# Kernel tuning notes

Hardware: AMD Instinct MI355X
Metric: run time of the kernel (lower is better)

## Reference

```python
import jax, jax.numpy as jnp
import numpy as np

TEMP = 0.02
KD_W = 1.0
VSD_W = 1.0
VLAD_W = 1.0
CON_W = 1.0
MSE_W = 1.0

B, SS, ST, DS, DT, V, NV, NT = 8, 96, 128, 1024, 2048, 32000, 32, 64


def hungarian(cost):
    # Shortest-augmenting-path assignment (e-maxx / Jonker-Volgenant style).
    # Square cost [n, n]; returns col_of_row so that row i matches column
    # col_of_row[i] with minimal total cost (same as scipy linear_sum_assignment).
    cost = np.asarray(cost, dtype=np.float64)
    n = cost.shape[0]
    INF = 1e18
    u = np.zeros(n + 1)
    v = np.zeros(n + 1)
    p = np.zeros(n + 1, dtype=np.int64)
    way = np.zeros(n + 1, dtype=np.int64)
    for i in range(1, n + 1):
        p[0] = i
        j0 = 0
        minv = np.full(n + 1, INF)
        used = np.zeros(n + 1, dtype=bool)
        while True:
            used[j0] = True
            i0 = p[j0]
            js = np.nonzero(~used)[0]
            js = js[js > 0]
            cur = cost[i0 - 1, js - 1] - u[i0] - v[js]
            upd = cur < minv[js]
            minv[js] = np.where(upd, cur, minv[js])
            way[js] = np.where(upd, j0, way[js])
            k = int(np.argmin(minv[js]))
            delta = minv[js][k]
            j1 = int(js[k])
            u[p[used]] += delta
            v[used] -= delta
            minv[~used] -= delta
            j0 = j1
            if p[j0] == 0:
                break
        while j0:
            j1 = int(way[j0])
            p[j0] = p[j1]
            j0 = j1
    col_of_row = np.zeros(n, dtype=np.int64)
    for j in range(1, n + 1):
        col_of_row[p[j] - 1] = j - 1
    return col_of_row


def _match(s_logits, t_logits):
    # Per-sample L1 (p=1 cdist) cost between teacher rows and student cols,
    # then Hungarian matching. Host-side loop is unavoidable (sequential
    # combinatorial algorithm), matching the original per-sample scipy loop.
    idx = []
    for b in range(s_logits.shape[0]):
        cost = np.abs(t_logits[b][:, None, :] - s_logits[b][None, :, :]).sum(-1)
        idx.append(hungarian(cost))
    return np.stack(idx)


def _cosine(a, b, eps=1e-8):
    # a: [B, M, D], b: [B, N, D] -> [B, M, N]; torch F.cosine_similarity semantics
    an = a / jnp.maximum(jnp.linalg.norm(a, axis=-1, keepdims=True), eps)
    bn = b / jnp.maximum(jnp.linalg.norm(b, axis=-1, keepdims=True), eps)
    return jnp.einsum('bmd,bnd->bmn', an, bn)


def setup_inputs() -> dict:
    key = jax.random.key(0)
    ks = jax.random.split(key, 12)
    f = jax.random.normal
    return {
        's_qry_reps': f(ks[0], (B, DS), jnp.float32),
        's_pos_reps': f(ks[1], (B, DS), jnp.float32),
        't_qry_reps': f(ks[2], (B, DT), jnp.float32),
        't_pos_reps': f(ks[3], (B, DT), jnp.float32),
        's_hidden_qry': f(ks[4], (B, SS, DS), jnp.float32),
        's_hidden_pos': f(ks[5], (B, SS, DS), jnp.float32),
        't_hidden_qry': f(ks[6], (B, ST, DT), jnp.float32),
        't_hidden_pos': f(ks[7], (B, ST, DT), jnp.float32),
        'W_s_lm': f(ks[8], (DS, V), jnp.float32) / np.float32(np.sqrt(DS)),
        'W_t_lm': f(ks[9], (DT, V), jnp.float32) / np.float32(np.sqrt(DT)),
        'W_proj': f(ks[10], (DT, DS), jnp.float32) / np.float32(np.sqrt(DT)),
        'b_proj': jnp.zeros((DS,), jnp.float32),
        'nv': NV,
        'nt': NT,
    }


def reference(s_qry_reps, s_pos_reps, t_qry_reps, t_pos_reps,
              s_hidden_qry, s_hidden_pos, t_hidden_qry, t_hidden_pos,
              W_s_lm, W_t_lm, W_proj, b_proj, nv, nt):
    Bn = s_qry_reps.shape[0]
    # 1) contrastive InfoNCE (world_size=1 -> gather is identity, target=arange)
    scores = (s_qry_reps @ s_pos_reps.T) / TEMP
    logp = jax.nn.log_softmax(scores, axis=-1)
    contrastive = -jnp.mean(jnp.diagonal(logp))
    # 2) MSE vs t2s-projected teacher reps
    mse = 0.5 * (jnp.mean((s_qry_reps - (t_qry_reps @ W_proj + b_proj)) ** 2)
                 + jnp.mean((s_pos_reps - (t_pos_reps @ W_proj + b_proj)) ** 2))
    # 3/4) VSD + VLAD over qry and pos sides stacked -> [2B, ...]
    s_hid = jnp.concatenate([s_hidden_qry, s_hidden_pos], axis=0)
    t_hid = jnp.concatenate([t_hidden_qry, t_hidden_pos], axis=0)
    St = t_hid.shape[1]
    sv = s_hid[:, :nv]                      # student vision tokens   [2B, Nv, DS]
    st = s_hid[:, nv:nv + nt]               # student text tokens     [2B, Nt, DS]
    tv = t_hid[:, St - nv - nt:St - nt]     # teacher vision tokens   [2B, Nv, DT]
    tt = t_hid[:, St - nt:]                 # teacher text tokens     [2B, Nt, DT]
    s_logits = jnp.einsum('bnd,dv->bnv', sv, W_s_lm)   # [2B, Nv, V]
    t_logits = jnp.einsum('bnd,dv->bnv', tv, W_t_lm)   # [2B, Nv, V]
    # Hungarian matching on detached logits (host side, like the original)
    idx = jnp.asarray(_match(np.asarray(s_logits), np.asarray(t_logits)))  # [2B, Nv]
    # VSD: MSE between matched student logits and teacher logits (t order = arange)
    s_logits_m = jnp.take_along_axis(s_logits, idx[:, :, None], axis=1)
    vsd = jnp.sum(jnp.mean((s_logits_m - t_logits) ** 2, axis=(1, 2)))
    # VLAD: smooth-L1 on vision->text cosine affinity maps
    sv_m = jnp.take_along_axis(sv, idx[:, :, None], axis=1)
    d = _cosine(sv_m, st) - _cosine(tv, tt)            # [2B, Nv, Nt]
    ad = jnp.abs(d)
    sl1 = jnp.where(ad < 1.0, 0.5 * d * d, ad - 0.5)
    vlad = jnp.sum(jnp.mean(sl1, axis=(1, 2)))
    distill = (VSD_W * vsd + VLAD_W * vlad) / Bn
    loss = CON_W * contrastive + MSE_W * mse + KD_W * distill
    return loss, contrastive, distill
```

## Files before the change

kernel.cpp:

```cpp
#include <hip/hip_runtime.h>
#include <math.h>

#define DS_ 1024
#define DT_ 2048
#define V_  32000
#define SS_ 96
#define ST_ 128


__device__ __forceinline__ float block_reduce_sum_256(float v) {
  __shared__ float tmp[4];
  #pragma unroll
  for (int off = 32; off; off >>= 1) v += __shfl_xor(v, off);
  const int wid = threadIdx.x >> 6;
  if ((threadIdx.x & 63) == 0) tmp[wid] = v;
  __syncthreads();
  if (threadIdx.x == 0) v = tmp[0] + tmp[1] + tmp[2] + tmp[3];
  return v;
}

__device__ __forceinline__ const float* s_base(int b, const float* s_hq, const float* s_hp) {
  return (b < 8) ? (s_hq + (size_t)b * SS_ * DS_) : (s_hp + (size_t)(b - 8) * SS_ * DS_);
}
__device__ __forceinline__ const float* t_base(int b, const float* t_hq, const float* t_hp) {
  return (b < 8) ? (t_hq + (size_t)b * ST_ * DT_) : (t_hp + (size_t)(b - 8) * ST_ * DT_);
}

__device__ __forceinline__ unsigned short f2bf(float x) {
  unsigned int u = __float_as_uint(x);
  u += 0x7fffu + ((u >> 16) & 1u);
  return (unsigned short)(u >> 16);
}
__device__ __forceinline__ float bf2f(unsigned short u) {
  return __uint_as_float(((unsigned int)u) << 16);
}

using bf16x8 = __attribute__((ext_vector_type(8))) short;
using f32x4  = __attribute__((ext_vector_type(4))) float;
using u16x4  = __attribute__((ext_vector_type(4))) unsigned short;

__device__ __forceinline__ void gll16(const void* g, void* l) {
  __builtin_amdgcn_global_load_lds((const __attribute__((address_space(1))) unsigned int*)g,
                                   (__attribute__((address_space(3))) unsigned int*)l, 16, 0, 0);
}

__device__ __forceinline__ unsigned int wave_umin_dpp(unsigned int r) {
  unsigned int t;
  t = (unsigned int)__builtin_amdgcn_update_dpp((int)r, (int)r, 0x111, 0xF, 0xF, false); r = r < t ? r : t;
  t = (unsigned int)__builtin_amdgcn_update_dpp((int)r, (int)r, 0x112, 0xF, 0xF, false); r = r < t ? r : t;
  t = (unsigned int)__builtin_amdgcn_update_dpp((int)r, (int)r, 0x114, 0xF, 0xF, false); r = r < t ? r : t;
  t = (unsigned int)__builtin_amdgcn_update_dpp((int)r, (int)r, 0x118, 0xF, 0xF, false); r = r < t ? r : t;
  t = (unsigned int)__builtin_amdgcn_update_dpp((int)r, (int)r, 0x142, 0xF, 0xF, false); r = r < t ? r : t;
  t = (unsigned int)__builtin_amdgcn_update_dpp((int)r, (int)r, 0x143, 0xF, 0xF, false); r = r < t ? r : t;
  return r;
}


__device__ __forceinline__ void scores_body(int blk, const float* __restrict__ sq,
                                            const float* __restrict__ sp,
                                            float* __restrict__ scores) {
  const int i = blk >> 3, j = blk & 7;
  float acc = 0.f;
  for (int k = threadIdx.x; k < DS_; k += 256)
    acc += sq[(size_t)i * DS_ + k] * sp[(size_t)j * DS_ + k];
  acc = block_reduce_sum_256(acc);
  if (threadIdx.x == 0) scores[i * 8 + j] = acc * 50.0f;
}

__device__ __forceinline__ void proj2_body(int kc, const float* __restrict__ t_qry,
                                           const float* __restrict__ t_pos,
                                           const float* __restrict__ Wp,
                                           float* __restrict__ proj,
                                           unsigned char* smem) {
  float (*tv)[64] = (float (*)[64])smem;
  const int tid = threadIdx.x;
  for (int s = tid; s < 16 * 64; s += 256) {
    const int zi = s >> 6, k = s & 63;
    const float* t = (zi >= 8) ? (t_pos + (size_t)(zi - 8) * DT_) : (t_qry + (size_t)zi * DT_);
    tv[zi][k] = t[kc * 64 + k];
  }
  __syncthreads();
  const int d4 = tid * 4;
  float4 acc[16];
  #pragma unroll
  for (int zi = 0; zi < 16; ++zi) acc[zi] = (float4){0.f, 0.f, 0.f, 0.f};
  for (int k = 0; k < 64; ++k) {
    const float4 w = *(const float4*)&Wp[(size_t)(kc * 64 + k) * DS_ + d4];
    #pragma unroll
    for (int zi = 0; zi < 16; ++zi) {
      const float t = tv[zi][k];
      acc[zi].x += t * w.x; acc[zi].y += t * w.y;
      acc[zi].z += t * w.z; acc[zi].w += t * w.w;
    }
  }
  #pragma unroll
  for (int zi = 0; zi < 16; ++zi) {
    float* p = proj + (size_t)zi * DS_ + d4;
    atomicAdd(&p[0], acc[zi].x); atomicAdd(&p[1], acc[zi].y);
    atomicAdd(&p[2], acc[zi].z); atomicAdd(&p[3], acc[zi].w);
  }
}

__device__ __forceinline__ void norms_body(int blk, const float* __restrict__ s_hq,
                                           const float* __restrict__ s_hp,
                                           const float* __restrict__ t_hq,
                                           const float* __restrict__ t_hp,
                                           float* __restrict__ invn) {
  const int b = blk / 192, t = blk % 192;
  const float* bs = s_base(b, s_hq, s_hp);
  const float* bt = t_base(b, t_hq, t_hp);
  const float* row;
  int K;
  float* out;
  if (t < 32)       { row = bs + (size_t)t * DS_;             K = DS_; out = invn + b * 32 + t; }
  else if (t < 96)  { row = bs + (size_t)t * DS_;             K = DS_; out = invn + 512 + b * 64 + (t - 32); }
  else if (t < 128) { row = bt + (size_t)(t - 96 + 32) * DT_;  K = DT_; out = invn + 1536 + b * 32 + (t - 96); }
  else              { row = bt + (size_t)(t - 128 + 64) * DT_; K = DT_; out = invn + 2048 + b * 64 + (t - 128); }
  float ss = 0.f;
  for (int k = threadIdx.x; k < K; k += 256) { const float x = row[k]; ss += x * x; }
  ss = block_reduce_sum_256(ss);
  if (threadIdx.x == 0) *out = 1.0f / fmaxf(sqrtf(ss), 1e-8f);
}

__device__ __forceinline__ void pack_as_body(int g, const float* __restrict__ s_hq,
                                             const float* __restrict__ s_hp,
                                             unsigned short* __restrict__ As) {
  const int b = g >> 5, i = g & 31;
  const float* src = s_base(b, s_hq, s_hp) + (size_t)i * DS_;
  const int k4 = threadIdx.x * 4;
  const float4 w = *(const float4*)&src[k4];
  u16x4 o; o[0] = f2bf(w.x); o[1] = f2bf(w.y); o[2] = f2bf(w.z); o[3] = f2bf(w.w);
  *(u16x4*)&As[(size_t)g * DS_ + k4] = o;
}

__device__ __forceinline__ void pack_at_body(int g, const float* __restrict__ t_hq,
                                             const float* __restrict__ t_hp,
                                             unsigned short* __restrict__ At) {
  const int b = g >> 5, i = g & 31;
  const float* src = t_base(b, t_hq, t_hp) + (size_t)(32 + i) * DT_;
  #pragma unroll
  for (int it = 0; it < 2; ++it) {
    const int k4 = (threadIdx.x + it * 256) * 4;
    const float4 w = *(const float4*)&src[k4];
    u16x4 o; o[0] = f2bf(w.x); o[1] = f2bf(w.y); o[2] = f2bf(w.z); o[3] = f2bf(w.w);
    *(u16x4*)&At[(size_t)g * DT_ + k4] = o;
  }
}

__device__ __forceinline__ void convw3_body(int id, const float* __restrict__ W,
                                            unsigned short* __restrict__ Wbt,
                                            int K, unsigned char* smem) {
  float* tile = (float*)smem;
  const int v0 = (id % 250) * 128, k0 = (id / 250) * 64;
  const int tid = threadIdx.x;
  const int wv = tid >> 6, lane = tid & 63;
  const int rowsel = lane >> 5, vlane = lane & 31;
  #pragma unroll
  for (int it = 0; it < 8; ++it) {
    const int w = it * 4 + wv;
    gll16(W + (size_t)(k0 + 2 * w + rowsel) * V_ + v0 + vlane * 4,
          tile + w * 256);
  }
  __syncthreads();
  #pragma unroll
  for (int it = 0; it < 4; ++it) {
    const int s = it * 256 + tid;
    const int v = s >> 3, ch = s & 7;
    unsigned int o[4];
    #pragma unroll
    for (int q = 0; q < 4; ++q) {
      const float a = tile[(ch * 8 + 2 * q) * 128 + v];
      const float b = tile[(ch * 8 + 2 * q + 1) * 128 + v];
      o[q] = (unsigned int)f2bf(a) | ((unsigned int)f2bf(b) << 16);
    }
    uint4 pk = {o[0], o[1], o[2], o[3]};
    *(uint4*)&Wbt[(size_t)(v0 + v) * K + k0 + ch * 8] = pk;
  }
}

__device__ __forceinline__ void dt_body(int id, const float* __restrict__ t_hq,
                                        const float* __restrict__ t_hp,
                                        float* __restrict__ dtd) {
  const int b = id >> 5, i = id & 31;
  const int wv = threadIdx.x >> 6, lane = threadIdx.x & 63;
  const float* bt = t_base(b, t_hq, t_hp);
  const float* a2p = bt + (size_t)(32 + i) * DT_;
  float a2[32];
  #pragma unroll
  for (int q = 0; q < 32; ++q) a2[q] = a2p[lane + 64 * q];
  for (int jj = 0; jj < 16; ++jj) {
    const int j = wv * 16 + jj;
    const float* b2 = bt + (size_t)(64 + j) * DT_;
    float dt = 0.f;
    #pragma unroll
    for (int q = 0; q < 32; ++q) dt += a2[q] * b2[lane + 64 * q];
    #pragma unroll
    for (int off = 32; off; off >>= 1) dt += __shfl_xor(dt, off);
    if (lane == 0) dtd[(b * 32 + i) * 64 + j] = dt;
  }
}

__device__ __forceinline__ void cs_body(int id, const float* __restrict__ s_hq,
                                        const float* __restrict__ s_hp,
                                        float* __restrict__ csd) {
  const int b = id >> 5, i = id & 31;
  const int wv = threadIdx.x >> 6, lane = threadIdx.x & 63;
  const float* bs = s_base(b, s_hq, s_hp);
  const float* a1p = bs + (size_t)i * DS_;
  float a1[16];
  #pragma unroll
  for (int q = 0; q < 16; ++q) a1[q] = a1p[lane + 64 * q];
  for (int jj = 0; jj < 16; ++jj) {
    const int j = wv * 16 + jj;
    const float* b1 = bs + (size_t)(32 + j) * DS_;
    float ds = 0.f;
    #pragma unroll
    for (int q = 0; q < 16; ++q) ds += a1[q] * b1[lane + 64 * q];
    #pragma unroll
    for (int off = 32; off; off >>= 1) ds += __shfl_xor(ds, off);
    if (lane == 0) csd[(b * 32 + i) * 64 + j] = ds;
  }
}

__device__ __forceinline__ void mse2_body(int blk, const float* __restrict__ s_qry,
                                          const float* __restrict__ s_pos,
                                          const float* __restrict__ proj,
                                          const float* __restrict__ bp,
                                          float* __restrict__ mse_acc) {
  const int z = blk >> 3, i = blk & 7;
  const float* s = (z ? s_pos : s_qry) + (size_t)i * DS_;
  const float* p = proj + ((size_t)z * 8 + i) * DS_;
  float ss = 0.f;
  for (int d = threadIdx.x; d < DS_; d += 256) {
    const float diff = s[d] - (p[d] + bp[d]);
    ss += diff * diff;
  }
  ss = block_reduce_sum_256(ss);
  if (threadIdx.x == 0) atomicAdd(mse_acc, ss);
}


template <int K>
__device__ __forceinline__ void gemm_body(int blk, int nwg,
                                          const unsigned short* __restrict__ A,
                                          const unsigned short* __restrict__ Wbt,
                                          unsigned short* __restrict__ Out,
                                          unsigned char* smem) {
  unsigned short* AldsB = (unsigned short*)smem;
  unsigned short* BldsB = (unsigned short*)(smem + 32768);
  const int q = nwg >> 3, r = nwg & 7;
  const int xcd = blk & 7, off = blk >> 3;
  const int sblk = (xcd < r ? xcd * (q + 1) : r * (q + 1) + (xcd - r) * q) + off;
  const int m0 = (sblk & 1) * 256;
  const int n0 = (sblk >> 1) * 128;
  const int tid = threadIdx.x;
  const int wv = tid >> 6, lane = tid & 63;
  const int lr = lane & 15, cc = lane >> 4;

  f32x4 acc[4][8];
  #pragma unroll
  for (int mf = 0; mf < 4; ++mf)
    #pragma unroll
    for (int nf = 0; nf < 8; ++nf) acc[mf][nf] = (f32x4){0.f, 0.f, 0.f, 0.f};

  constexpr int NT = K / 32;

  auto stage = [&](int kt, int buf) {
    #pragma unroll
    for (int it = 0; it < 4; ++it) {
      const int slot = it * 256 + tid;
      const int row = slot >> 2, cs = slot & 3;
      gll16(A + (size_t)(m0 + row) * K + kt * 32 + ((cs ^ ((row >> 1) & 3)) << 3),
            AldsB + (size_t)buf * 8192 + (size_t)(it * 256 + wv * 64) * 8);
    }
    #pragma unroll
    for (int it = 0; it < 2; ++it) {
      const int slot = it * 256 + tid;
      const int row = slot >> 2, cs = slot & 3;
      gll16(Wbt + (size_t)(n0 + row) * K + kt * 32 + ((cs ^ ((row >> 1) & 3)) << 3),
            BldsB + (size_t)buf * 4096 + (size_t)(it * 256 + wv * 64) * 8);
    }
  };

  stage(0, 0);
  if (NT > 1) stage(1, 1);
  for (int kt = 0; kt < NT; ++kt) {
    const int cur = kt & 1;
    if (kt >= 1 && kt + 1 < NT) stage(kt + 1, cur ^ 1);
    if (kt + 1 < NT) asm volatile("s_waitcnt vmcnt(6)" ::: "memory");
    else             asm volatile("s_waitcnt vmcnt(0)" ::: "memory");
    asm volatile("s_barrier" ::: "memory");
    bf16x8 af[4];
    #pragma unroll
    for (int mf = 0; mf < 4; ++mf) {
      const int row = wv * 64 + mf * 16 + lr;
      af[mf] = *(const bf16x8*)(AldsB + cur * 8192 + row * 32 + ((cc ^ ((row >> 1) & 3)) << 3));
    }
    __builtin_amdgcn_s_setprio(1);
    #pragma unroll
    for (int nf = 0; nf < 8; ++nf) {
      const int vr = nf * 16 + lr;
      const bf16x8 bfr = *(const bf16x8*)(BldsB + cur * 4096 + vr * 32 + ((cc ^ ((vr >> 1) & 3)) << 3));
      #pragma unroll
      for (int mf = 0; mf < 4; ++mf)
        acc[mf][nf] = __builtin_amdgcn_mfma_f32_16x16x32_bf16(af[mf], bfr, acc[mf][nf], 0, 0, 0);
    }
    __builtin_amdgcn_s_setprio(0);
    asm volatile("s_barrier" ::: "memory");
  }

  unsigned short* Olds = AldsB;
  #pragma unroll
  for (int h = 0; h < 2; ++h) {
    if (h) __syncthreads();
    #pragma unroll
    for (int mf = 0; mf < 4; ++mf)
      #pragma unroll
      for (int nf4 = 0; nf4 < 4; ++nf4) {
        const int nf = h * 4 + nf4;
        #pragma unroll
        for (int q2 = 0; q2 < 4; ++q2) {
          const int row = wv * 64 + mf * 16 + (lane >> 4) * 4 + q2;
          const int col = nf4 * 16 + lr;
          Olds[row * 64 + (col ^ (((row >> 2) & 3) << 4))] = f2bf(acc[mf][nf][q2]);
        }
      }
    __syncthreads();
    #pragma unroll
    for (int it = 0; it < 4; ++it) {
      const int slot = it * 256 + tid;
      const int row = slot >> 3, c2 = slot & 7;
      const uint4 pk = *(const uint4*)&Olds[row * 64 + ((c2 ^ (((row >> 2) & 3) << 1)) << 3)];
      *(uint4*)&Out[(size_t)(m0 + row) * V_ + n0 + h * 64 + c2 * 8] = pk;
    }
  }
}


__global__ __launch_bounds__(256) void fused_l0_kernel(const float* __restrict__ s_qry,
                                                       const float* __restrict__ s_pos,
                                                       const float* __restrict__ t_qry,
                                                       const float* __restrict__ t_pos,
                                                       const float* __restrict__ s_hq,
                                                       const float* __restrict__ s_hp,
                                                       const float* __restrict__ t_hq,
                                                       const float* __restrict__ t_hp,
                                                       const float* __restrict__ Ws,
                                                       const float* __restrict__ Wt,
                                                       const float* __restrict__ Wp,
                                                       float* __restrict__ scores,
                                                       float* __restrict__ proj,
                                                       float* __restrict__ invn,
                                                       unsigned short* __restrict__ As,
                                                       unsigned short* __restrict__ At,
                                                       unsigned short* __restrict__ Wsb,
                                                       unsigned short* __restrict__ Wtb,
                                                       float* __restrict__ csd,
                                                       float* __restrict__ dtd) {
  __shared__ __align__(16) unsigned char smem[32768];
  const int blk = blockIdx.x;
  if (blk < 8000)          convw3_body(blk, Wt, Wtb, DT_, smem);
  else if (blk < 12000)    convw3_body(blk - 8000, Ws, Wsb, DS_, smem);
  else if (blk < 12064)    scores_body(blk - 12000, s_qry, s_pos, scores);
  else if (blk < 12096)    proj2_body(blk - 12064, t_qry, t_pos, Wp, proj, smem);
  else if (blk < 15168)    norms_body(blk - 12096, s_hq, s_hp, t_hq, t_hp, invn);
  else if (blk < 15680)    pack_as_body(blk - 15168, s_hq, s_hp, As);
  else if (blk < 16192)    pack_at_body(blk - 15680, t_hq, t_hp, At);
  else if (blk < 16704)    cs_body(blk - 16192, s_hq, s_hp, csd);
  else                     dt_body(blk - 16704, t_hq, t_hp, dtd);
}

__global__ __launch_bounds__(256) void fused_l1_kernel(const unsigned short* __restrict__ As,
                                                       const unsigned short* __restrict__ Wsb,
                                                       unsigned short* __restrict__ Sg,
                                                       const unsigned short* __restrict__ At,
                                                       const unsigned short* __restrict__ Wtb,
                                                       unsigned short* __restrict__ Tg,
                                                       const float* __restrict__ s_qry,
                                                       const float* __restrict__ s_pos,
                                                       const float* __restrict__ proj,
                                                       const float* __restrict__ bp,
                                                       float* __restrict__ mse_acc) {
  __shared__ __align__(16) unsigned char smem[49152];
  const int blk = blockIdx.x;
  if (blk < 500)            gemm_body<DT_>(blk, 500, At, Wtb, Tg, smem);
  else if (blk < 1000)      gemm_body<DS_>(blk - 500, 500, As, Wsb, Sg, smem);
  else                      mse2_body(blk - 1000, s_qry, s_pos, proj, bp, mse_acc);
}


#define CPV 500
#define CPP 508

__global__ __launch_bounds__(256) void cost_pairs_kernel(const unsigned short* __restrict__ Sg,
                                                         const unsigned short* __restrict__ Tg,
                                                         float* __restrict__ cost1,
                                                         float* __restrict__ cost2) {
  __shared__ __align__(16) unsigned short Sl[32 * CPP];
  __shared__ __align__(16) unsigned short Tl[32 * CPP];
  const int b = blockIdx.x >> 6, sl = blockIdx.x & 63;
  const int v0 = sl * CPV;
  const int tid = threadIdx.x;

  for (int s = tid; s < 32 * 125; s += 256) {
    const int r = s / 125, c = s % 125;
    *(u16x4*)&Sl[r * CPP + c * 4] = *(const u16x4*)&Sg[(size_t)(b * 32 + r) * V_ + v0 + c * 4];
    *(u16x4*)&Tl[r * CPP + c * 4] = *(const u16x4*)&Tg[(size_t)(b * 32 + r) * V_ + v0 + c * 4];
  }
  __syncthreads();

  const int i = tid >> 3, j4 = (tid & 7) * 4;
  float a1[4] = {0.f, 0.f, 0.f, 0.f}, a2[4] = {0.f, 0.f, 0.f, 0.f};
  for (int v = 0; v < CPV; v += 4) {
    const u16x4 t4 = *(const u16x4*)&Tl[i * CPP + v];
    float tf[4];
    #pragma unroll
    for (int q = 0; q < 4; ++q) tf[q] = bf2f(t4[q]);
    #pragma unroll
    for (int jj = 0; jj < 4; ++jj) {
      const u16x4 s4 = *(const u16x4*)&Sl[(j4 + jj) * CPP + v];
      #pragma unroll
      for (int q = 0; q < 4; ++q) {
        const float d = tf[q] - bf2f(s4[q]);
        a1[jj] += fabsf(d);
        a2[jj] += d * d;
      }
    }
  }
  #pragma unroll
  for (int jj = 0; jj < 4; ++jj) {
    atomicAdd(&cost1[(size_t)b * 1024 + i * 32 + j4 + jj], a1[jj]);
    atomicAdd(&cost2[(size_t)b * 1024 + i * 32 + j4 + jj], a2[jj]);
  }
}


__global__ __launch_bounds__(256) void hung_vlad_kernel(const float* __restrict__ cost1,
                                                        const float* __restrict__ cost2,
                                                        const float* __restrict__ invn,
                                                        const float* __restrict__ csd,
                                                        const float* __restrict__ dtd,
                                                        float* __restrict__ vsd_acc,
                                                        float* __restrict__ vlad_acc) {
  const int b = blockIdx.x;
  const int tid = threadIdx.x;
  const float INF = __int_as_float(0x7f800000);
  __shared__ float C[32 * 33];
  __shared__ float u_lds[33];
  __shared__ int idx_lds[32];

  for (int s = tid; s < 1024; s += 256) {
    const int r = s >> 5, c = s & 31;
    C[r * 33 + c] = cost1[(size_t)b * 1024 + s];
  }
  if (tid == 0) u_lds[0] = 0.f;
  __syncthreads();
  if (tid < 32) {
    float m = C[tid * 33];
    for (int j = 1; j < 32; ++j) m = fminf(m, C[tid * 33 + j]);
    u_lds[tid + 1] = m;
  }
  __syncthreads();

  if (tid < 64) {
    const int lane = tid;
    const bool isj = (lane >= 1 && lane <= 32);
    const int cix = isj ? (lane - 1) : 0;

    float v = 0.f;
    if (isj) {
      float m = INF;
      for (int i = 0; i < 32; ++i) m = fminf(m, C[i * 33 + cix] - u_lds[i + 1]);
      v = m;
    }

    int p = 0;
    unsigned int assigned = 0;
    for (int i = 1; i <= 32; ++i) {
      const float ui = u_lds[i];
      const bool zero = isj && (p == 0) && ((C[(i - 1) * 33 + cix] - ui) == v);
      const unsigned long long tie = __ballot(zero);
      if (tie) {
        const int j1 = __ffsll(tie) - 1;
        if (lane == j1) p = i;
        assigned |= (1u << (i - 1));
      }
    }

    for (int i = 1; i <= 32; ++i) {
      if (assigned & (1u << (i - 1))) continue;
      if (lane == 0) p = i;
      float minv = INF;
      int way = 0;
      int used = 0;
      int j0 = 0;
      float ui0 = u_lds[i];
      float crow = C[(i - 1) * 33 + cix];
      while (true) {
        if (lane == j0) used = 1;
        float val = INF;
        if (isj && !used) {
          const float cur = crow - ui0 - v;
          if (cur < minv) { minv = cur; way = j0; }
          val = minv;
        }
        const unsigned int rb = wave_umin_dpp(__float_as_uint(val));
        const unsigned int minb = (unsigned int)__builtin_amdgcn_readlane((int)rb, 63);
        const float delta = __uint_as_float(minb);
        const unsigned long long tie = __ballot(__float_as_uint(val) == minb);
        const int j1 = __ffsll(tie) - 1;
        const int i0n = __builtin_amdgcn_readlane(p, j1);
        const float ui0n = u_lds[i0n];
        const int nri = (i0n >= 1 ? i0n : 1) - 1;
        const float cnext = C[nri * 33 + cix];
        if (used) {
          u_lds[p] += delta;
          v -= delta;
        } else {
          minv -= delta;
        }
        j0 = j1;
        if (i0n == 0) break;
        ui0 = ui0n;
        crow = cnext;
      }
      while (j0) {
        const int j1 = __builtin_amdgcn_readlane(way, j0);
        const int pv = __builtin_amdgcn_readlane(p, j1);
        if (lane == j0) p = pv;
        j0 = j1;
      }
    }
    float term = 0.f;
    if (isj) {
      idx_lds[p - 1] = lane - 1;
      term = cost2[(size_t)b * 1024 + (p - 1) * 32 + (lane - 1)];
    }
    #pragma unroll
    for (int off = 32; off; off >>= 1) term += __shfl_xor(term, off);
    if (lane == 0) atomicAdd(vsd_acc, term);
  }
  __syncthreads();

  float local = 0.f;
  #pragma unroll
  for (int w = 0; w < 8; ++w) {
    const int cell = tid * 8 + w;
    const int i = cell >> 6, j = cell & 63;
    const int is = idx_lds[i];
    const float cs = csd[(b * 32 + is) * 64 + j] * invn[b * 32 + is] * invn[512 + b * 64 + j];
    const float ct = dtd[(b * 32 + i) * 64 + j] * invn[1536 + b * 32 + i] * invn[2048 + b * 64 + j];
    const float d = cs - ct;
    const float ad = fabsf(d);
    local += (ad < 1.f) ? 0.5f * d * d : ad - 0.5f;
  }
  local = block_reduce_sum_256(local);
  if (tid == 0) atomicAdd(vlad_acc, local);
}


__global__ __launch_bounds__(64) void final_kernel(const float* __restrict__ scores,
                                                   const float* __restrict__ accs,
                                                   float* __restrict__ out) {
  const int lane = threadIdx.x;
  float ci = 0.f;
  if (lane < 8) {
    float m = -1e30f;
    for (int j = 0; j < 8; ++j) m = fmaxf(m, scores[lane * 8 + j]);
    float sum = 0.f;
    for (int j = 0; j < 8; ++j) sum += expf(scores[lane * 8 + j] - m);
    const float lse = m + logf(sum);
    ci = scores[lane * 8 + lane] - lse;
  }
  #pragma unroll
  for (int off = 32; off; off >>= 1) ci += __shfl_xor(ci, off);
  if (lane == 0) {
    const float contrastive = -ci / 8.0f;
    const float mse = accs[0] / 16384.0f;
    const float vsd = accs[1] / 1024000.0f;
    const float vlad = accs[2] / 2048.0f;
    const float distill = (vsd + vlad) / 8.0f;
    out[0] = contrastive + mse + distill;
    out[1] = contrastive;
    out[2] = distill;
  }
}


extern "C" void kernel_launch(void* const* d_in, const int* in_sizes, int n_in,
                              void* d_out, int out_size, void* d_ws, size_t ws_size,
                              hipStream_t stream) {
  const float* s_qry = (const float*)d_in[0];
  const float* s_pos = (const float*)d_in[1];
  const float* t_qry = (const float*)d_in[2];
  const float* t_pos = (const float*)d_in[3];
  const float* s_hq  = (const float*)d_in[4];
  const float* s_hp  = (const float*)d_in[5];
  const float* t_hq  = (const float*)d_in[6];
  const float* t_hp  = (const float*)d_in[7];
  const float* Ws    = (const float*)d_in[8];
  const float* Wt    = (const float*)d_in[9];
  const float* Wp    = (const float*)d_in[10];
  const float* bp    = (const float*)d_in[11];

  float* ws     = (float*)d_ws;
  float* scores = ws;
  float* cost1  = ws + 64;
  float* cost2  = ws + 16448;
  float* invn   = ws + 32832;
  float* accs   = ws + 35904;
  float* proj   = ws + 35908;
  float* csd    = ws + 52292;
  float* dtd    = ws + 85060;
  const size_t small_bytes = (size_t)52292 * 4;

  const size_t As_off = 524288;
  const size_t At_off = As_off + (size_t)512 * DS_ * 2;
  const size_t Ws_off = At_off + (size_t)512 * DT_ * 2;
  const size_t Wt_off = Ws_off + (size_t)V_ * DS_ * 2;
  const size_t Sg_off = Wt_off + (size_t)V_ * DT_ * 2;
  const size_t Tg_off = Sg_off + (size_t)512 * V_ * 2;
  const size_t req2   = Tg_off + (size_t)512 * V_ * 2;

  hipMemsetAsync(d_ws, 0, small_bytes, stream);

  if (ws_size >= req2) {
    unsigned short* As  = (unsigned short*)((char*)d_ws + As_off);
    unsigned short* At  = (unsigned short*)((char*)d_ws + At_off);
    unsigned short* Wsb = (unsigned short*)((char*)d_ws + Ws_off);
    unsigned short* Wtb = (unsigned short*)((char*)d_ws + Wt_off);
    unsigned short* Sg  = (unsigned short*)((char*)d_ws + Sg_off);
    unsigned short* Tg  = (unsigned short*)((char*)d_ws + Tg_off);

    fused_l0_kernel<<<17216, 256, 0, stream>>>(s_qry, s_pos, t_qry, t_pos,
                                               s_hq, s_hp, t_hq, t_hp,
                                               Ws, Wt, Wp, scores, proj, invn,
                                               As, At, Wsb, Wtb, csd, dtd);

    fused_l1_kernel<<<1016, 256, 0, stream>>>(As, Wsb, Sg, At, Wtb, Tg,
                                              s_qry, s_pos, proj, bp, accs + 0);

    cost_pairs_kernel<<<16 * 64, 256, 0, stream>>>(Sg, Tg, cost1, cost2);

    hung_vlad_kernel<<<16, 256, 0, stream>>>(cost1, cost2, invn, csd, dtd,
                                             accs + 1, accs + 2);
    final_kernel<<<1, 64, 0, stream>>>(scores, accs, (float*)d_out);
  }
}
```

Measured before the change: 432.3 us.

## Widen weight-conversion tiles and move independent side work into GEMM launch

The fp32-to-bf16 weight transpose now handles 256 vocab columns per block instead of 128. This halves the block count and gives each thread one column with eight contiguous 16-byte stores, at the cost of a 64KB shared tile. The scores, norms, cs and dt work, which does not feed the GEMMs, moves from the first fused launch into the second. There it can fill idle CUs alongside the 1000 GEMM blocks, shortening the conversion-bound first kernel. The 64KB of shared memory per block may reduce occupancy in the conversion kernel.

```diff
diff --git a/kernel.cpp b/kernel.cpp
--- a/kernel.cpp
+++ b/kernel.cpp
@@ -147,30 +147,27 @@
   }
 }
 
-__device__ __forceinline__ void convw3_body(int id, const float* __restrict__ W,
+__device__ __forceinline__ void convw4_body(int id, const float* __restrict__ W,
                                             unsigned short* __restrict__ Wbt,
                                             int K, unsigned char* smem) {
   float* tile = (float*)smem;
-  const int v0 = (id % 250) * 128, k0 = (id / 250) * 64;
+  const int v0 = (id % 125) * 256, k0 = (id / 125) * 64;
   const int tid = threadIdx.x;
   const int wv = tid >> 6, lane = tid & 63;
-  const int rowsel = lane >> 5, vlane = lane & 31;
-  #pragma unroll
-  for (int it = 0; it < 8; ++it) {
-    const int w = it * 4 + wv;
-    gll16(W + (size_t)(k0 + 2 * w + rowsel) * V_ + v0 + vlane * 4,
-          tile + w * 256);
+  #pragma unroll
+  for (int r = 0; r < 16; ++r) {
+    const int k = wv * 16 + r;
+    gll16(W + (size_t)(k0 + k) * V_ + v0 + lane * 4, tile + k * 256);
   }
   __syncthreads();
-  #pragma unroll
-  for (int it = 0; it < 4; ++it) {
-    const int s = it * 256 + tid;
-    const int v = s >> 3, ch = s & 7;
+  const int v = tid;
+  #pragma unroll
+  for (int ch = 0; ch < 8; ++ch) {
     unsigned int o[4];
     #pragma unroll
     for (int q = 0; q < 4; ++q) {
-      const float a = tile[(ch * 8 + 2 * q) * 128 + v];
-      const float b = tile[(ch * 8 + 2 * q + 1) * 128 + v];
+      const float a = tile[(ch * 8 + 2 * q) * 256 + v];
+      const float b = tile[(ch * 8 + 2 * q + 1) * 256 + v];
       o[q] = (unsigned int)f2bf(a) | ((unsigned int)f2bf(b) << 16);
     }
     uint4 pk = {o[0], o[1], o[2], o[3]};
@@ -337,9 +334,7 @@
 }
 
 
-__global__ __launch_bounds__(256) void fused_l0_kernel(const float* __restrict__ s_qry,
-                                                       const float* __restrict__ s_pos,
-                                                       const float* __restrict__ t_qry,
+__global__ __launch_bounds__(256) void fused_l0_kernel(const float* __restrict__ t_qry,
                                                        const float* __restrict__ t_pos,
                                                        const float* __restrict__ s_hq,
                                                        const float* __restrict__ s_hp,
@@ -348,26 +343,18 @@
                                                        const float* __restrict__ Ws,
                                                        const float* __restrict__ Wt,
                                                        const float* __restrict__ Wp,
-                                                       float* __restrict__ scores,
                                                        float* __restrict__ proj,
-                                                       float* __restrict__ invn,
                                                        unsigned short* __restrict__ As,
                                                        unsigned short* __restrict__ At,
                                                        unsigned short* __restrict__ Wsb,
-                                                       unsigned short* __restrict__ Wtb,
-                                                       float* __restrict__ csd,
-                                                       float* __restrict__ dtd) {
-  __shared__ __align__(16) unsigned char smem[32768];
+                                                       unsigned short* __restrict__ Wtb) {
+  __shared__ __align__(16) unsigned char smem[65536];
   const int blk = blockIdx.x;
-  if (blk < 8000)          convw3_body(blk, Wt, Wtb, DT_, smem);
-  else if (blk < 12000)    convw3_body(blk - 8000, Ws, Wsb, DS_, smem);
-  else if (blk < 12064)    scores_body(blk - 12000, s_qry, s_pos, scores);
-  else if (blk < 12096)    proj2_body(blk - 12064, t_qry, t_pos, Wp, proj, smem);
-  else if (blk < 15168)    norms_body(blk - 12096, s_hq, s_hp, t_hq, t_hp, invn);
-  else if (blk < 15680)    pack_as_body(blk - 15168, s_hq, s_hp, As);
-  else if (blk < 16192)    pack_at_body(blk - 15680, t_hq, t_hp, At);
-  else if (blk < 16704)    cs_body(blk - 16192, s_hq, s_hp, csd);
-  else                     dt_body(blk - 16704, t_hq, t_hp, dtd);
+  if (blk < 4000)          convw4_body(blk, Wt, Wtb, DT_, smem);
+  else if (blk < 6000)     convw4_body(blk - 4000, Ws, Wsb, DS_, smem);
+  else if (blk < 6512)     pack_as_body(blk - 6000, s_hq, s_hp, As);
+  else if (blk < 7024)     pack_at_body(blk - 6512, t_hq, t_hp, At);
+  else                     proj2_body(blk - 7024, t_qry, t_pos, Wp, proj, smem);
 }
 
 __global__ __launch_bounds__(256) void fused_l1_kernel(const unsigned short* __restrict__ As,
@@ -378,14 +365,26 @@
                                                        unsigned short* __restrict__ Tg,
                                                        const float* __restrict__ s_qry,
                                                        const float* __restrict__ s_pos,
+                                                       const float* __restrict__ s_hq,
+                                                       const float* __restrict__ s_hp,
+                                                       const float* __restrict__ t_hq,
+                                                       const float* __restrict__ t_hp,
                                                        const float* __restrict__ proj,
                                                        const float* __restrict__ bp,
-                                                       float* __restrict__ mse_acc) {
+                                                       float* __restrict__ mse_acc,
+                                                       float* __restrict__ scores,
+                                                       float* __restrict__ invn,
+                                                       float* __restrict__ csd,
+                                                       float* __restrict__ dtd) {
   __shared__ __align__(16) unsigned char smem[49152];
   const int blk = blockIdx.x;
   if (blk < 500)            gemm_body<DT_>(blk, 500, At, Wtb, Tg, smem);
   else if (blk < 1000)      gemm_body<DS_>(blk - 500, 500, As, Wsb, Sg, smem);
-  else                      mse2_body(blk - 1000, s_qry, s_pos, proj, bp, mse_acc);
+  else if (blk < 1016)      mse2_body(blk - 1000, s_qry, s_pos, proj, bp, mse_acc);
+  else if (blk < 1080)      scores_body(blk - 1016, s_qry, s_pos, scores);
+  else if (blk < 4152)      norms_body(blk - 1080, s_hq, s_hp, t_hq, t_hp, invn);
+  else if (blk < 4664)      cs_body(blk - 4152, s_hq, s_hp, csd);
+  else                      dt_body(blk - 4664, t_hq, t_hp, dtd);
 }
 
 
@@ -632,13 +631,12 @@
     unsigned short* Sg  = (unsigned short*)((char*)d_ws + Sg_off);
     unsigned short* Tg  = (unsigned short*)((char*)d_ws + Tg_off);
 
-    fused_l0_kernel<<<17216, 256, 0, stream>>>(s_qry, s_pos, t_qry, t_pos,
-                                               s_hq, s_hp, t_hq, t_hp,
-                                               Ws, Wt, Wp, scores, proj, invn,
-                                               As, At, Wsb, Wtb, csd, dtd);
-
-    fused_l1_kernel<<<1016, 256, 0, stream>>>(As, Wsb, Sg, At, Wtb, Tg,
-                                              s_qry, s_pos, proj, bp, accs + 0);
+    fused_l0_kernel<<<7056, 256, 0, stream>>>(t_qry, t_pos, s_hq, s_hp, t_hq, t_hp,
+                                              Ws, Wt, Wp, proj, As, At, Wsb, Wtb);
+
+    fused_l1_kernel<<<5176, 256, 0, stream>>>(As, Wsb, Sg, At, Wtb, Tg,
+                                              s_qry, s_pos, s_hq, s_hp, t_hq, t_hp,
+                                              proj, bp, accs + 0, scores, invn, csd, dtd);
 
     cost_pairs_kernel<<<16 * 64, 256, 0, stream>>>(Sg, Tg, cost1, cost2);
 
```

Result: slower. 483.8 us (+11.9%).
